# Performance work log

Measured on AMD Instinct MI355X. Metric: run time of the kernel, lower is better.

The kernel has to match this reference:

```python
import jax, jax.numpy as jnp
import numpy as np

ATT, WEMB, VIEW, ADIM, EMB = 312, 512, 16, 2048, 2048
B = 2048
IN = ATT + WEMB + VIEW * WEMB  # 9016; output_dim defaults to input_dim
EPS = 1e-8  # torch cosine_similarity eps


def setup_inputs() -> dict:
    key = jax.random.key(0)
    ks = jax.random.split(key, 8)
    s = 0.02
    return {
        "x": jax.random.normal(ks[0], (B, IN), dtype=jnp.float32),
        "Wq": s * jax.random.normal(ks[1], (WEMB, ADIM), dtype=jnp.float32),
        "bq": jnp.zeros((ADIM,), jnp.float32),
        "Wk": s * jax.random.normal(ks[2], (WEMB, ADIM), dtype=jnp.float32),
        "bk": jnp.zeros((ADIM,), jnp.float32),
        "Wv": s * jax.random.normal(ks[3], (WEMB, ADIM), dtype=jnp.float32),
        "bv": jnp.zeros((ADIM,), jnp.float32),
        "Wm": s * jax.random.normal(ks[4], (ATT + ADIM, EMB), dtype=jnp.float32),
        "bm": jnp.zeros((EMB,), jnp.float32),
        "Wd1": s * jax.random.normal(ks[5], (EMB, 4096), dtype=jnp.float32),
        "bd1": jnp.zeros((4096,), jnp.float32),
        "Wd2": s * jax.random.normal(ks[6], (4096, IN), dtype=jnp.float32),
        "bd2": jnp.zeros((IN,), jnp.float32),
    }


def reference(x, Wq, bq, Wk, bk, Wv, bv, Wm, bm, Wd1, bd1, Wd2, bd2):
    att_emb = x[:, :ATT]                                   # [B, 312]
    desc_emb = x[:, ATT:ATT + WEMB]                        # [B, 512]
    gpt_emb = x[:, ATT + WEMB:].reshape(x.shape[0], -1, WEMB)  # [B, V, 512]

    # q is the same projected desc for every view (expand before linear)
    q = desc_emb @ Wq + bq                                 # [B, A]
    k = jnp.einsum("bvw,wa->bva", gpt_emb, Wk) + bk        # [B, V, A]
    v = jnp.einsum("bvw,wa->bva", gpt_emb, Wv) + bv        # [B, V, A]

    # cosed score: cosine similarity * L2 distance
    dot = jnp.einsum("bva,ba->bv", k, q)                   # [B, V]
    qn = jnp.maximum(jnp.linalg.norm(q, axis=-1), EPS)     # [B]
    kn = jnp.maximum(jnp.linalg.norm(k, axis=-1), EPS)     # [B, V]
    cs = dot / (qn[:, None] * kn)
    ed = jnp.linalg.norm(q[:, None, :] - k, axis=-1)       # [B, V]
    attn = jax.nn.softmax(cs * ed, axis=-1)                # [B, V]

    # torch.matmul([B,V], [B,V,A]) -> [B,B,A]; .mean(dim=1) averages over the
    # attn-batch axis, i.e. fused[j] = mean_b(attn[b]) @ v[j]. Compute the
    # mathematically identical form without the BxBxA intermediate.
    attn_mean = attn.mean(axis=0)                          # [V]
    fused = jnp.einsum("v,bva->ba", attn_mean, v)          # [B, A]

    z = jax.nn.relu(jnp.concatenate([att_emb, fused], axis=1) @ Wm + bm)  # [B, EMB]
    h = jax.nn.relu(z @ Wd1 + bd1)                          # [B, 4096]
    return h @ Wd2 + bd2                                    # [B, IN]
```

## Files before the change

### kernel.cpp

```cpp
#include <hip/hip_runtime.h>


typedef __bf16 bf16x8 __attribute__((ext_vector_type(8)));
typedef float  f32x4  __attribute__((ext_vector_type(4)));
typedef unsigned short u16;

#define ATT   312
#define WEMB  512
#define VIEW  16
#define ADIM  2048
#define EMB   2048
#define BATCH 2048
#define INDIM 9016
#define KCAT  2360
#define KCATP 2432
#define NOUT  9016
#define NOUTP 9216

__device__ __forceinline__ u16 f2bf(float f) {
  unsigned u = __builtin_bit_cast(unsigned, f);
  u += 0x7FFFu + ((u >> 16) & 1u);
  return (u16)(u >> 16);
}

__device__ __forceinline__ void gl_lds16(const u16* g, u16* l) {
  __builtin_amdgcn_global_load_lds((const __attribute__((address_space(1))) void*)g,
                                   (__attribute__((address_space(3))) void*)l, 16, 0, 0);
}

__global__ void castx_k(const float* __restrict__ x, u16* __restrict__ cc,
                        u16* __restrict__ desc, u16* __restrict__ gpt) {
  const int b = blockIdx.x, t = threadIdx.x;
  const float4* row = (const float4*)(x + (size_t)b * INDIM);
  for (int c = t; c < INDIM / 4; c += 256) {
    float4 v = row[c];
    ushort4 o = make_ushort4(f2bf(v.x), f2bf(v.y), f2bf(v.z), f2bf(v.w));
    if (c < ATT / 4)                 *(ushort4*)&cc[(size_t)b * KCATP + c * 4] = o;
    else if (c < (ATT + WEMB) / 4)   *(ushort4*)&desc[(size_t)b * WEMB + (c - ATT / 4) * 4] = o;
    else                             *(ushort4*)&gpt[(size_t)b * (VIEW * WEMB) + (c - (ATT + WEMB) / 4) * 4] = o;
  }
  if (t < (KCATP - KCAT) / 4) {
    *(ushort4*)&cc[(size_t)b * KCATP + KCAT + t * 4] = make_ushort4(0, 0, 0, 0);
  }
}

struct TcDesc { const float* src; u16* dst; int K, N, Kp, Np, ntx, base; };
struct TcArgs { TcDesc d[6]; };

__global__ void transcast6_k(TcArgs A) {
  __shared__ float tile[64][65];
  int mi = 0;
  const int bid = blockIdx.x;
#pragma unroll
  for (int i = 1; i < 6; ++i) if (bid >= A.d[i].base) mi = i;
  const TcDesc& D = A.d[mi];
  const int local = bid - D.base;
  const int n0 = (local % D.ntx) * 64, k0 = (local / D.ntx) * 64;
  const int t = threadIdx.x;
  const int tr = t >> 4, tc4 = (t & 15) * 4;
#pragma unroll
  for (int i = 0; i < 4; ++i) {
    const int k = k0 + tr + i * 16;
    float v0 = 0.f, v1 = 0.f, v2 = 0.f, v3 = 0.f;
    if (k < D.K) {
      const int n = n0 + tc4;
      const float* p = D.src + (size_t)k * D.N + n;
      if (n + 3 < D.N) { float4 v = *(const float4*)p; v0 = v.x; v1 = v.y; v2 = v.z; v3 = v.w; }
      else {
        if (n + 0 < D.N) v0 = p[0];
        if (n + 1 < D.N) v1 = p[1];
        if (n + 2 < D.N) v2 = p[2];
        if (n + 3 < D.N) v3 = p[3];
      }
    }
    tile[tr + i * 16][tc4 + 0] = v0;
    tile[tr + i * 16][tc4 + 1] = v1;
    tile[tr + i * 16][tc4 + 2] = v2;
    tile[tr + i * 16][tc4 + 3] = v3;
  }
  __syncthreads();
#pragma unroll
  for (int i = 0; i < 4; ++i) {
    const int rn = tr + i * 16;
    const int n = n0 + rn;
    const int kk = k0 + tc4;
    if (n < D.Np && kk < D.Kp) {
      const bool nv = (n < D.N);
      ushort4 o = make_ushort4(f2bf(nv ? tile[tc4 + 0][rn] : 0.f),
                               f2bf(nv ? tile[tc4 + 1][rn] : 0.f),
                               f2bf(nv ? tile[tc4 + 2][rn] : 0.f),
                               f2bf(nv ? tile[tc4 + 3][rn] : 0.f));
      *(ushort4*)&D.dst[(size_t)n * D.Kp + kk] = o;
    }
  }
}

__device__ __forceinline__ void stage_half(const u16* __restrict__ src, int ld,
                                           u16* dst, int wave, int lane) {
#pragma unroll
  for (int j = 0; j < 2; ++j) {
    const int s = wave * 2 + j;
    const int r = ((s >> 1) << 4) + (lane >> 2);
    const int c = ((s & 1) << 5) +
                  (((lane & 3) << 3) ^ (((lane >> 5) & 1) << 4));
    gl_lds16(src + (long)r * ld + c, dst + s * 512 + (lane << 3));
  }
}

#define BAR   __builtin_amdgcn_s_barrier()
#define LGKM0 asm volatile("s_waitcnt lgkmcnt(0)" ::: "memory")
#define VM6   asm volatile("s_waitcnt vmcnt(6)" ::: "memory")
#define VM4   asm volatile("s_waitcnt vmcnt(4)" ::: "memory")
#define VM0   asm volatile("s_waitcnt vmcnt(0)" ::: "memory")

#define RDA(bufo, lo, hi) do { _Pragma("unroll") for (int mf = (lo); mf <= (hi); ++mf) \
  _Pragma("unroll") for (int kk = 0; kk < 2; ++kk) \
    a[mf][kk] = *(const bf16x8*)&lds[(bufo) + aoff0 + (mf * 2 + kk) * 512]; } while (0)
#define RDB(bufo, lo, hi) do { _Pragma("unroll") for (int nf = (lo); nf <= (hi); ++nf) \
  _Pragma("unroll") for (int kk = 0; kk < 2; ++kk) \
    b[nf][kk] = *(const bf16x8*)&lds[(bufo) + boff0 + nf * 1024 + kk * 512]; } while (0)
#define QUAD(qm, qn) do { __builtin_amdgcn_s_setprio(1); \
  _Pragma("unroll") for (int m4 = 0; m4 < 4; ++m4) \
  _Pragma("unroll") for (int n2 = 0; n2 < 2; ++n2) \
  _Pragma("unroll") for (int kk = 0; kk < 2; ++kk) \
    acc[(qm) * 4 + m4][(qn) * 2 + n2] = __builtin_amdgcn_mfma_f32_16x16x32_bf16( \
        a[(qm) * 4 + m4][kk], b[(qn) * 2 + n2][kk], acc[(qm) * 4 + m4][(qn) * 2 + n2], 0, 0, 0); \
  __builtin_amdgcn_s_setprio(0); } while (0)

template <int MODE, bool RELU>
__global__ __launch_bounds__(512, 2)
void gemm256(const u16* __restrict__ A, const u16* __restrict__ BT,
             const float* __restrict__ bias, int K, int Nreal,
             float* __restrict__ dstF, u16* __restrict__ dstH,
             float* __restrict__ PF, int ldc,
             const float* __restrict__ qbuf, float* __restrict__ dotb,
             float* __restrict__ kn2b, int mt, int nt, int fastm,
             int ks, int kl) {
  __shared__ alignas(16) u16 lds[65536];
  const int nwg = mt * nt * ks;
  const int xcd = blockIdx.x & 7, idx = blockIdx.x >> 3;
  const int qq = nwg >> 3, rr = nwg & 7;
  const int wg = (xcd < rr ? xcd * (qq + 1) : rr * (qq + 1) + (xcd - rr) * qq) + idx;
  const int ksl = wg % ks;
  const int rem = wg / ks;
  int tm, tn;
  if (fastm) { tm = rem % mt; tn = rem / mt; } else { tn = rem % nt; tm = rem / nt; }

  const int tid = threadIdx.x;
  const int wave = tid >> 6, lane = tid & 63;
  const long m0 = (long)tm * 256, n0 = (long)tn * 256;
  const int wm = wave >> 2, wn = wave & 3;
  const u16* Ab = A + m0 * K + (long)ksl * kl;
  const u16* Bb = BT + n0 * K + (long)ksl * kl;

  f32x4 acc[8][4] = {};
  bf16x8 a[8][2], b[4][2];
  const int LP = (lane & 15) * 32 + ((((lane >> 4) << 3)) ^ (((lane >> 3) & 1) << 4));
  const int aoff0 = wm * 8192 + LP;
  const int boff0 = 16384 + (wn >> 1) * 8192 + (wn & 1) * 4096 + LP;
  const int NT = kl >> 6;

  stage_half(Ab,                K, &lds[0],     wave, lane);
  stage_half(Ab + 128 * K,      K, &lds[8192],  wave, lane);
  stage_half(Bb,                K, &lds[16384], wave, lane);
  stage_half(Bb + 128 * K,      K, &lds[24576], wave, lane);
  stage_half(Ab + 64,           K, &lds[32768], wave, lane);
  stage_half(Ab + 128 * K + 64, K, &lds[40960], wave, lane);
  stage_half(Bb + 64,           K, &lds[49152], wave, lane);
  VM6; BAR;

  const int iters = NT >> 1;
  for (int i = 0; i < iters; ++i) {
    const int t0 = 2 * i;
    const bool nl = (i < iters - 1);
    RDA(0, 0, 3); RDB(0, 0, 1);
    stage_half(Bb + 128 * K + (t0 + 1) * 64, K, &lds[57344], wave, lane);
    BAR; LGKM0; QUAD(0, 0); BAR;
    RDA(0, 4, 7);
    BAR; LGKM0; QUAD(1, 0); BAR;
    RDB(0, 2, 3);
    if (nl) stage_half(Ab + (t0 + 2) * 64, K, &lds[0], wave, lane);
    BAR; LGKM0; QUAD(0, 1); BAR;
    if (nl) stage_half(Ab + 128 * K + (t0 + 2) * 64, K, &lds[8192], wave, lane);
    BAR; QUAD(1, 1);
    if (nl) { VM4; } else { VM0; }
    BAR;
    RDA(32768, 0, 3); RDB(32768, 0, 1);
    if (nl) stage_half(Bb + (t0 + 2) * 64, K, &lds[16384], wave, lane);
    BAR; LGKM0; QUAD(0, 0); BAR;
    RDA(32768, 4, 7);
    if (nl) stage_half(Bb + 128 * K + (t0 + 2) * 64, K, &lds[24576], wave, lane);
    BAR; LGKM0; QUAD(1, 0); BAR;
    RDB(32768, 2, 3);
    if (nl) stage_half(Ab + (t0 + 3) * 64, K, &lds[32768], wave, lane);
    BAR; LGKM0; QUAD(0, 1); BAR;
    if (nl) {
      stage_half(Ab + 128 * K + (t0 + 3) * 64, K, &lds[40960], wave, lane);
      stage_half(Bb + (t0 + 3) * 64, K, &lds[49152], wave, lane);
    }
    BAR; QUAD(1, 1);
    if (nl) VM6;
    BAR;
  }

  const int lr = lane >> 4, lc = lane & 15;
  if (MODE == 2) {
#pragma unroll
    for (int mf = 0; mf < 8; ++mf) {
#pragma unroll
      for (int r = 0; r < 4; ++r) {
        const long grow = m0 + wm * 128 + mf * 16 + lr * 4 + r;
        const long bb = grow >> 4;
        float ds = 0.f, ks2 = 0.f;
#pragma unroll
        for (int nf = 0; nf < 4; ++nf) {
          const long col = n0 + wn * 64 + nf * 16 + lc;
          float kv = acc[mf][nf][r] + bias[col];
          ds += kv * qbuf[bb * ADIM + col];
          ks2 += kv * kv;
        }
#pragma unroll
        for (int m = 1; m < 16; m <<= 1) {
          ds += __shfl_xor(ds, m, 64);
          ks2 += __shfl_xor(ks2, m, 64);
        }
        if (lc == 0) {
          atomicAdd(&dotb[grow], ds);
          atomicAdd(&kn2b[grow], ks2);
        }
      }
    }
  } else if (MODE == 4) {
    float* base = (ksl == 0) ? dstF : PF;
#pragma unroll
    for (int mf = 0; mf < 8; ++mf) {
#pragma unroll
      for (int nf = 0; nf < 4; ++nf) {
        const long col = n0 + wn * 64 + nf * 16 + lc;
        if (col < Nreal) {
          const float bv_ = (ksl == 0) ? bias[col] : 0.f;
#pragma unroll
          for (int r = 0; r < 4; ++r) {
            const long row = m0 + wm * 128 + mf * 16 + lr * 4 + r;
            base[row * (long)ldc + col] = acc[mf][nf][r] + bv_;
          }
        }
      }
    }
  } else {
#pragma unroll
    for (int mf = 0; mf < 8; ++mf) {
#pragma unroll
      for (int nf = 0; nf < 4; ++nf) {
        const long col = n0 + wn * 64 + nf * 16 + lc;
        if (col < Nreal) {
          const float bv_ = bias[col];
#pragma unroll
          for (int r = 0; r < 4; ++r) {
            const long row = m0 + wm * 128 + mf * 16 + lr * 4 + r;
            float v = acc[mf][nf][r] + bv_;
            if (RELU) v = fmaxf(v, 0.f);
            if (MODE == 0) dstF[row * (long)ldc + col] = v;
            else           dstH[row * (long)ldc + col] = f2bf(v);
          }
        }
      }
    }
  }
}

__global__ void addf_k(float* __restrict__ out, const float* __restrict__ p) {
  const size_t i = ((size_t)blockIdx.x * 256 + threadIdx.x) * 4;
  float4 a = *(float4*)&out[i];
  float4 b = *(const float4*)&p[i];
  a.x += b.x; a.y += b.y; a.z += b.z; a.w += b.w;
  *(float4*)&out[i] = a;
}

template <int MODE, bool RELU>
__global__ __launch_bounds__(256, 2)
void gemm_bt(const u16* __restrict__ A, const u16* __restrict__ BT,
             const float* __restrict__ bias, int K, int Nreal,
             float* __restrict__ dstF, u16* __restrict__ dstH, int ldc,
             int mt, int nt, int fastm) {
  __shared__ alignas(16) u16 Ash[128 * 64];
  __shared__ alignas(16) u16 Bsh[128 * 64];
  const int nwg = mt * nt;
  const int xcd = blockIdx.x & 7, idx = blockIdx.x >> 3;
  const int qq = nwg >> 3, rr = nwg & 7;
  const int wg = (xcd < rr ? xcd * (qq + 1) : rr * (qq + 1) + (xcd - rr) * qq) + idx;
  int tm, tn;
  if (fastm) { tm = wg % mt; tn = wg / mt; } else { tn = wg % nt; tm = wg / nt; }

  const int tid = threadIdx.x;
  const int wave = tid >> 6, lane = tid & 63;
  const long m0 = (long)tm * 128;
  const long n0 = (long)tn * 128;
  const int wm = wave >> 1, wnn = wave & 1;
  f32x4 acc[4][4] = {};

  const int srow = (wave << 5) + (lane >> 3);
  const int scol = (lane & 7) << 3;

  for (int k0 = 0; k0 < K; k0 += 64) {
    __syncthreads();
#pragma unroll
    for (int i = 0; i < 4; ++i) {
      const int r = srow + i * 8;
      gl_lds16(A + (m0 + r) * (long)K + k0 + scol, &Ash[r * 64 + scol]);
      gl_lds16(BT + (n0 + r) * (long)K + k0 + scol, &Bsh[r * 64 + scol]);
    }
    __syncthreads();
#pragma unroll
    for (int kb = 0; kb < 2; ++kb) {
      bf16x8 af[4], bfv[4];
#pragma unroll
      for (int f = 0; f < 4; ++f) {
        af[f]  = *(const bf16x8*)&Ash[(wm * 64 + f * 16 + (lane & 15)) * 64 + kb * 32 + (lane >> 4) * 8];
        bfv[f] = *(const bf16x8*)&Bsh[(wnn * 64 + f * 16 + (lane & 15)) * 64 + kb * 32 + (lane >> 4) * 8];
      }
#pragma unroll
      for (int mf = 0; mf < 4; ++mf)
#pragma unroll
        for (int nf = 0; nf < 4; ++nf)
          acc[mf][nf] = __builtin_amdgcn_mfma_f32_16x16x32_bf16(af[mf], bfv[nf], acc[mf][nf], 0, 0, 0);
    }
  }

  const int lr = lane >> 4, lc = lane & 15;
#pragma unroll
  for (int mf = 0; mf < 4; ++mf) {
#pragma unroll
    for (int nf = 0; nf < 4; ++nf) {
      const long col = n0 + wnn * 64 + nf * 16 + lc;
      if (col < Nreal) {
        const float bv_ = bias[col];
#pragma unroll
        for (int r = 0; r < 4; ++r) {
          const long row = m0 + wm * 64 + mf * 16 + lr * 4 + r;
          float v = acc[mf][nf][r] + bv_;
          if (RELU) v = fmaxf(v, 0.f);
          if (MODE == 0) dstF[row * (long)ldc + col] = v;
          else           dstH[row * (long)ldc + col] = f2bf(v);
        }
      }
    }
  }
}

__global__ void qnorm_k(const float* __restrict__ q, float* __restrict__ qn2) {
  const int b = blockIdx.x, t = threadIdx.x;
  const float4* row = (const float4*)(q + (size_t)b * ADIM);
  float s = 0.f;
#pragma unroll
  for (int i = 0; i < 2; ++i) {
    float4 v = row[t + i * 256];
    s += v.x * v.x + v.y * v.y + v.z * v.z + v.w * v.w;
  }
#pragma unroll
  for (int m = 1; m < 64; m <<= 1) s += __shfl_xor(s, m, 64);
  __shared__ float wsum[4];
  if ((t & 63) == 0) wsum[t >> 6] = s;
  __syncthreads();
  if (t == 0) qn2[b] = wsum[0] + wsum[1] + wsum[2] + wsum[3];
}

__global__ void attn_k(const float* __restrict__ dotb, const float* __restrict__ kn2b,
                       const float* __restrict__ qn2, float* __restrict__ asum) {
  const int b = blockIdx.x * 256 + threadIdx.x;
  const int lane = threadIdx.x & 63;
  const float q2 = qn2[b];
  const float qn = fmaxf(sqrtf(q2), 1e-8f);
  float lg[VIEW];
  float mx = -1e30f;
#pragma unroll
  for (int v = 0; v < VIEW; ++v) {
    const float d = dotb[b * VIEW + v], k2 = kn2b[b * VIEW + v];
    const float kn = fmaxf(sqrtf(k2), 1e-8f);
    const float cs = d / (qn * kn);
    const float ed = sqrtf(fmaxf(q2 - 2.f * d + k2, 0.f));
    lg[v] = cs * ed;
    mx = fmaxf(mx, lg[v]);
  }
  float s = 0.f;
#pragma unroll
  for (int v = 0; v < VIEW; ++v) { lg[v] = expf(lg[v] - mx); s += lg[v]; }
  const float inv = 1.f / s;
#pragma unroll
  for (int v = 0; v < VIEW; ++v) {
    float aa = lg[v] * inv;
#pragma unroll
    for (int m = 1; m < 64; m <<= 1) aa += __shfl_xor(aa, m, 64);
    if (lane == 0) atomicAdd(&asum[v], aa);
  }
}

__global__ void gtilde_k(const u16* __restrict__ gpt, const float* __restrict__ asum,
                         u16* __restrict__ g) {
  const int b = blockIdx.x, t = threadIdx.x;
  float am[VIEW];
#pragma unroll
  for (int v = 0; v < VIEW; ++v) am[v] = asum[v] * (1.f / (float)BATCH);
  float s[8] = {};
  const u16* gx = gpt + (size_t)b * (VIEW * WEMB) + t * 8;
#pragma unroll
  for (int v = 0; v < VIEW; ++v) {
    bf16x8 gv = *(const bf16x8*)&gx[v * WEMB];
#pragma unroll
    for (int j = 0; j < 8; ++j) s[j] += am[v] * (float)gv[j];
  }
  ushort4 o0, o1;
  o0 = make_ushort4(f2bf(s[0]), f2bf(s[1]), f2bf(s[2]), f2bf(s[3]));
  o1 = make_ushort4(f2bf(s[4]), f2bf(s[5]), f2bf(s[6]), f2bf(s[7]));
  *(ushort4*)&g[(size_t)b * WEMB + t * 8] = o0;
  *(ushort4*)&g[(size_t)b * WEMB + t * 8 + 4] = o1;
}

extern "C" void kernel_launch(void* const* d_in, const int* in_sizes, int n_in,
                              void* d_out, int out_size, void* d_ws, size_t ws_size,
                              hipStream_t stream) {
  const float* x   = (const float*)d_in[0];
  const float* Wq  = (const float*)d_in[1];
  const float* bq  = (const float*)d_in[2];
  const float* Wk  = (const float*)d_in[3];
  const float* bk  = (const float*)d_in[4];
  const float* Wv  = (const float*)d_in[5];
  const float* bv  = (const float*)d_in[6];
  const float* Wm  = (const float*)d_in[7];
  const float* bm  = (const float*)d_in[8];
  const float* Wd1 = (const float*)d_in[9];
  const float* bd1 = (const float*)d_in[10];
  const float* Wd2 = (const float*)d_in[11];
  const float* bd2 = (const float*)d_in[12];
  float* out = (float*)d_out;

  char* ws = (char*)d_ws;
  size_t off = 0;
  auto alloc = [&](size_t bytes) -> void* {
    void* p = ws + off;
    off = (off + bytes + 255) & ~(size_t)255;
    return p;
  };
  u16* WqT  = (u16*)alloc((size_t)ADIM * WEMB * 2);
  u16* WkT  = (u16*)alloc((size_t)ADIM * WEMB * 2);
  u16* WvT  = (u16*)alloc((size_t)ADIM * WEMB * 2);
  u16* WmT  = (u16*)alloc((size_t)EMB * KCATP * 2);
  u16* Wd1T = (u16*)alloc((size_t)4096 * EMB * 2);
  u16* Wd2T = (u16*)alloc((size_t)NOUTP * 4096 * 2);
  u16* desc = (u16*)alloc((size_t)BATCH * WEMB * 2);
  u16* gpt  = (u16*)alloc((size_t)BATCH * VIEW * WEMB * 2);
  u16* cc   = (u16*)alloc((size_t)BATCH * KCATP * 2);
  float* q    = (float*)alloc((size_t)BATCH * ADIM * 4);
  float* qn2  = (float*)alloc((size_t)BATCH * 4);
  float* stats = (float*)alloc((size_t)(BATCH * VIEW * 2 + 64) * 4);
  float* dotb = stats;
  float* kn2b = stats + BATCH * VIEW;
  float* asum = stats + BATCH * VIEW * 2;
  u16* gt = (u16*)alloc((size_t)BATCH * WEMB * 2);
  u16* z  = (u16*)alloc((size_t)BATCH * EMB * 2);
  (void)alloc((size_t)1 << 20);
  u16* h  = (u16*)alloc((size_t)BATCH * 4096 * 2);
  if (off > ws_size) return;
  float* Pout = (float*)desc;

  hipMemsetAsync(stats, 0, (size_t)(BATCH * VIEW * 2 + 64) * 4, stream);

  castx_k<<<BATCH, 256, 0, stream>>>(x, cc, desc, gpt);

  TcArgs ta;
  int base = 0;
  auto setd = [&](int i, const float* s, u16* d, int K, int N, int Kp, int Np) {
    ta.d[i] = TcDesc{s, d, K, N, Kp, Np, (Np + 63) / 64, base};
    base += ((Np + 63) / 64) * ((Kp + 63) / 64);
  };
  setd(0, Wq, WqT, WEMB, ADIM, WEMB, ADIM);
  setd(1, Wk, WkT, WEMB, ADIM, WEMB, ADIM);
  setd(2, Wv, WvT, WEMB, ADIM, WEMB, ADIM);
  setd(3, Wm, WmT, KCAT, EMB, KCATP, EMB);
  setd(4, Wd1, Wd1T, EMB, 4096, EMB, 4096);
  setd(5, Wd2, Wd2T, 4096, NOUT, 4096, NOUTP);
  transcast6_k<<<base, 256, 0, stream>>>(ta);

  gemm_bt<0, false><<<16 * 16, 256, 0, stream>>>(
      desc, WqT, bq, WEMB, ADIM, q, nullptr, ADIM, BATCH / 128, ADIM / 128, 0);
  qnorm_k<<<BATCH, 256, 0, stream>>>(q, qn2);
  gemm256<2, false><<<128 * 8, 512, 0, stream>>>(
      gpt, WkT, bk, WEMB, ADIM, nullptr, nullptr, nullptr, 0, q, dotb, kn2b,
      BATCH * VIEW / 256, ADIM / 256, 0, 1, WEMB);
  attn_k<<<BATCH / 256, 256, 0, stream>>>(dotb, kn2b, qn2, asum);
  gtilde_k<<<BATCH, 64, 0, stream>>>(gpt, asum, gt);
  gemm_bt<1, false><<<16 * 16, 256, 0, stream>>>(
      gt, WvT, bv, WEMB, ADIM, nullptr, cc + ATT, KCATP, BATCH / 128, ADIM / 128, 0);
  gemm_bt<1, true><<<16 * 16, 256, 0, stream>>>(
      cc, WmT, bm, KCATP, EMB, nullptr, z, EMB, BATCH / 128, EMB / 128, 0);
  gemm256<1, true><<<8 * 16, 512, 0, stream>>>(
      z, Wd1T, bd1, EMB, 4096, nullptr, h, nullptr, 4096, nullptr, nullptr, nullptr,
      BATCH / 256, 4096 / 256, 1, 1, EMB);
  gemm256<4, false><<<8 * 36 * 2, 512, 0, stream>>>(
      h, Wd2T, bd2, 4096, NOUT, out, nullptr, Pout, NOUT, nullptr, nullptr, nullptr,
      BATCH / 256, NOUTP / 256, 1, 2, 2048);
  addf_k<<<(BATCH * NOUT) / 1024, 256, 0, stream>>>(out, Pout);
}
```

Measured before the change: 690.4 us.

## Rebalance decoder GEMM work splits: split-K Wd1, tail-only split-K for Wd2

The first decoder GEMM (z@Wd1) now runs as a 2-way split-K over 256 workgroups instead of 128, writing bf16 partials plus an fp32 partial buffer that a new kernel sums, applies ReLU to, and casts. The second decoder GEMM drops its uniform 2-way split-K. It now computes the 256 full-K tiles for columns below 8192 directly, and splits only the ragged tail column block 8-way in K, reducing it with a small tail kernel. This removes the full-output partial add pass and balances workgroups against the CU count. In exchange it adds an extra kernel, a bf16-rounded intermediate for h's first partial, and larger partial buffers.

```diff
diff --git a/kernel.cpp b/kernel.cpp
--- a/kernel.cpp
+++ b/kernel.cpp
@@ -21,6 +21,10 @@
   unsigned u = __builtin_bit_cast(unsigned, f);
   u += 0x7FFFu + ((u >> 16) & 1u);
   return (u16)(u >> 16);
+}
+__device__ __forceinline__ float bf2f(u16 b) {
+  unsigned u = (unsigned)b << 16;
+  return __builtin_bit_cast(float, u);
 }
 
 __device__ __forceinline__ void gl_lds16(const u16* g, u16* l) {
@@ -127,38 +131,55 @@
         a[(qm) * 4 + m4][kk], b[(qn) * 2 + n2][kk], acc[(qm) * 4 + m4][(qn) * 2 + n2], 0, 0, 0); \
   __builtin_amdgcn_s_setprio(0); } while (0)
 
-template <int MODE, bool RELU>
+template <int MODE>
 __global__ __launch_bounds__(512, 2)
 void gemm256(const u16* __restrict__ A, const u16* __restrict__ BT,
              const float* __restrict__ bias, int K, int Nreal,
              float* __restrict__ dstF, u16* __restrict__ dstH,
              float* __restrict__ PF, int ldc,
              const float* __restrict__ qbuf, float* __restrict__ dotb,
-             float* __restrict__ kn2b, int mt, int nt, int fastm,
-             int ks, int kl) {
+             float* __restrict__ kn2b, int mt, int nt, int fastm) {
   __shared__ alignas(16) u16 lds[65536];
-  const int nwg = mt * nt * ks;
-  const int xcd = blockIdx.x & 7, idx = blockIdx.x >> 3;
-  const int qq = nwg >> 3, rr = nwg & 7;
-  const int wg = (xcd < rr ? xcd * (qq + 1) : rr * (qq + 1) + (xcd - rr) * qq) + idx;
-  const int ksl = wg % ks;
-  const int rem = wg / ks;
-  int tm, tn;
-  if (fastm) { tm = rem % mt; tn = rem / mt; } else { tn = rem % nt; tm = rem / nt; }
+  int tm, tn, ksl = 0, kloc = K;
+  long koff = 0;
+  if (MODE == 5) {
+    if ((int)blockIdx.x < 256) {
+      const int w = ((blockIdx.x & 7) << 5) + (blockIdx.x >> 3);
+      tm = w & 7; tn = w >> 3;
+    } else {
+      const int b2 = blockIdx.x - 256;
+      const int w = ((b2 & 7) << 5) + (b2 >> 3);
+      const int tile = w >> 3; ksl = w & 7;
+      tm = tile & 7; tn = 32 + (tile >> 3);
+      kloc = 512; koff = (long)ksl * 512;
+    }
+  } else if (MODE == 6) {
+    const int w = ((blockIdx.x & 7) << 5) + (blockIdx.x >> 3);
+    ksl = w & 1;
+    const int tile = w >> 1;
+    tm = tile & 7; tn = tile >> 3;
+    kloc = K >> 1; koff = (long)ksl * kloc;
+  } else {
+    const int nwg = mt * nt;
+    const int xcd = blockIdx.x & 7, idx = blockIdx.x >> 3;
+    const int qq = nwg >> 3, rr = nwg & 7;
+    const int wg = (xcd < rr ? xcd * (qq + 1) : rr * (qq + 1) + (xcd - rr) * qq) + idx;
+    if (fastm) { tm = wg % mt; tn = wg / mt; } else { tn = wg % nt; tm = wg / nt; }
+  }
 
   const int tid = threadIdx.x;
   const int wave = tid >> 6, lane = tid & 63;
   const long m0 = (long)tm * 256, n0 = (long)tn * 256;
   const int wm = wave >> 2, wn = wave & 3;
-  const u16* Ab = A + m0 * K + (long)ksl * kl;
-  const u16* Bb = BT + n0 * K + (long)ksl * kl;
+  const u16* Ab = A + m0 * K + koff;
+  const u16* Bb = BT + n0 * K + koff;
 
   f32x4 acc[8][4] = {};
   bf16x8 a[8][2], b[4][2];
   const int LP = (lane & 15) * 32 + ((((lane >> 4) << 3)) ^ (((lane >> 3) & 1) << 4));
   const int aoff0 = wm * 8192 + LP;
   const int boff0 = 16384 + (wn >> 1) * 8192 + (wn & 1) * 4096 + LP;
-  const int NT = kl >> 6;
+  const int NT = kloc >> 6;
 
   stage_half(Ab,                K, &lds[0],     wave, lane);
   stage_half(Ab + 128 * K,      K, &lds[8192],  wave, lane);
@@ -230,51 +251,83 @@
         }
       }
     }
-  } else if (MODE == 4) {
-    float* base = (ksl == 0) ? dstF : PF;
+  } else if (MODE == 5) {
+    if (ksl == 0) {
+#pragma unroll
+      for (int mf = 0; mf < 8; ++mf) {
+#pragma unroll
+        for (int nf = 0; nf < 4; ++nf) {
+          const long col = n0 + wn * 64 + nf * 16 + lc;
+          if (col < Nreal) {
+            const float bv_ = bias[col];
+#pragma unroll
+            for (int r = 0; r < 4; ++r) {
+              const long row = m0 + wm * 128 + mf * 16 + lr * 4 + r;
+              dstF[row * (long)ldc + col] = acc[mf][nf][r] + bv_;
+            }
+          }
+        }
+      }
+    } else {
+      float* pt = PF + (long)(ksl - 1) * BATCH * 1024;
+#pragma unroll
+      for (int mf = 0; mf < 8; ++mf) {
+#pragma unroll
+        for (int nf = 0; nf < 4; ++nf) {
+          const long col = n0 + wn * 64 + nf * 16 + lc;
+#pragma unroll
+          for (int r = 0; r < 4; ++r) {
+            const long row = m0 + wm * 128 + mf * 16 + lr * 4 + r;
+            pt[row * 1024 + (col - 8192)] = acc[mf][nf][r];
+          }
+        }
+      }
+    }
+  } else {
 #pragma unroll
     for (int mf = 0; mf < 8; ++mf) {
 #pragma unroll
       for (int nf = 0; nf < 4; ++nf) {
         const long col = n0 + wn * 64 + nf * 16 + lc;
-        if (col < Nreal) {
-          const float bv_ = (ksl == 0) ? bias[col] : 0.f;
-#pragma unroll
-          for (int r = 0; r < 4; ++r) {
-            const long row = m0 + wm * 128 + mf * 16 + lr * 4 + r;
-            base[row * (long)ldc + col] = acc[mf][nf][r] + bv_;
-          }
-        }
-      }
-    }
-  } else {
-#pragma unroll
-    for (int mf = 0; mf < 8; ++mf) {
-#pragma unroll
-      for (int nf = 0; nf < 4; ++nf) {
-        const long col = n0 + wn * 64 + nf * 16 + lc;
-        if (col < Nreal) {
-          const float bv_ = bias[col];
-#pragma unroll
-          for (int r = 0; r < 4; ++r) {
-            const long row = m0 + wm * 128 + mf * 16 + lr * 4 + r;
-            float v = acc[mf][nf][r] + bv_;
-            if (RELU) v = fmaxf(v, 0.f);
-            if (MODE == 0) dstF[row * (long)ldc + col] = v;
-            else           dstH[row * (long)ldc + col] = f2bf(v);
-          }
-        }
-      }
-    }
-  }
-}
-
-__global__ void addf_k(float* __restrict__ out, const float* __restrict__ p) {
-  const size_t i = ((size_t)blockIdx.x * 256 + threadIdx.x) * 4;
-  float4 a = *(float4*)&out[i];
-  float4 b = *(const float4*)&p[i];
-  a.x += b.x; a.y += b.y; a.z += b.z; a.w += b.w;
-  *(float4*)&out[i] = a;
+        const float bv_ = bias[col];
+#pragma unroll
+        for (int r = 0; r < 4; ++r) {
+          const long row = m0 + wm * 128 + mf * 16 + lr * 4 + r;
+          if (ksl == 0) dstH[row * (long)ldc + col] = f2bf(acc[mf][nf][r] + bv_);
+          else          PF[row * (long)ldc + col] = acc[mf][nf][r];
+        }
+      }
+    }
+  }
+}
+
+__global__ void relucast2_k(u16* __restrict__ h, const float* __restrict__ ph) {
+  const size_t i = ((size_t)blockIdx.x * 256 + threadIdx.x) * 8;
+  bf16x8 hv = *(const bf16x8*)&h[i];
+  float4 pa = *(const float4*)&ph[i];
+  float4 pb = *(const float4*)&ph[i + 4];
+  ushort4 o0 = make_ushort4(f2bf(fmaxf((float)hv[0] + pa.x, 0.f)),
+                            f2bf(fmaxf((float)hv[1] + pa.y, 0.f)),
+                            f2bf(fmaxf((float)hv[2] + pa.z, 0.f)),
+                            f2bf(fmaxf((float)hv[3] + pa.w, 0.f)));
+  ushort4 o1 = make_ushort4(f2bf(fmaxf((float)hv[4] + pb.x, 0.f)),
+                            f2bf(fmaxf((float)hv[5] + pb.y, 0.f)),
+                            f2bf(fmaxf((float)hv[6] + pb.z, 0.f)),
+                            f2bf(fmaxf((float)hv[7] + pb.w, 0.f)));
+  *(ushort4*)&h[i] = o0;
+  *(ushort4*)&h[i + 4] = o1;
+}
+
+__global__ void tailred_k(float* __restrict__ out, const float* __restrict__ pt) {
+  const int i = blockIdx.x * 256 + threadIdx.x;
+  const int row = i / 206, c = (i % 206) * 4;
+  float4 acc = *(float4*)&out[(size_t)row * NOUT + 8192 + c];
+#pragma unroll
+  for (int s = 0; s < 7; ++s) {
+    float4 p = *(const float4*)&pt[(size_t)s * BATCH * 1024 + (size_t)row * 1024 + c];
+    acc.x += p.x; acc.y += p.y; acc.z += p.z; acc.w += p.w;
+  }
+  *(float4*)&out[(size_t)row * NOUT + 8192 + c] = acc;
 }
 
 template <int MODE, bool RELU>
@@ -458,10 +511,10 @@
   float* asum = stats + BATCH * VIEW * 2;
   u16* gt = (u16*)alloc((size_t)BATCH * WEMB * 2);
   u16* z  = (u16*)alloc((size_t)BATCH * EMB * 2);
-  (void)alloc((size_t)1 << 20);
   u16* h  = (u16*)alloc((size_t)BATCH * 4096 * 2);
   if (off > ws_size) return;
-  float* Pout = (float*)desc;
+  float* Ph    = (float*)desc;
+  float* Ptail = (float*)desc;
 
   hipMemsetAsync(stats, 0, (size_t)(BATCH * VIEW * 2 + 64) * 4, stream);
 
@@ -484,20 +537,21 @@
   gemm_bt<0, false><<<16 * 16, 256, 0, stream>>>(
       desc, WqT, bq, WEMB, ADIM, q, nullptr, ADIM, BATCH / 128, ADIM / 128, 0);
   qnorm_k<<<BATCH, 256, 0, stream>>>(q, qn2);
-  gemm256<2, false><<<128 * 8, 512, 0, stream>>>(
+  gemm256<2><<<128 * 8, 512, 0, stream>>>(
       gpt, WkT, bk, WEMB, ADIM, nullptr, nullptr, nullptr, 0, q, dotb, kn2b,
-      BATCH * VIEW / 256, ADIM / 256, 0, 1, WEMB);
+      BATCH * VIEW / 256, ADIM / 256, 0);
   attn_k<<<BATCH / 256, 256, 0, stream>>>(dotb, kn2b, qn2, asum);
   gtilde_k<<<BATCH, 64, 0, stream>>>(gpt, asum, gt);
   gemm_bt<1, false><<<16 * 16, 256, 0, stream>>>(
       gt, WvT, bv, WEMB, ADIM, nullptr, cc + ATT, KCATP, BATCH / 128, ADIM / 128, 0);
   gemm_bt<1, true><<<16 * 16, 256, 0, stream>>>(
       cc, WmT, bm, KCATP, EMB, nullptr, z, EMB, BATCH / 128, EMB / 128, 0);
-  gemm256<1, true><<<8 * 16, 512, 0, stream>>>(
-      z, Wd1T, bd1, EMB, 4096, nullptr, h, nullptr, 4096, nullptr, nullptr, nullptr,
-      BATCH / 256, 4096 / 256, 1, 1, EMB);
-  gemm256<4, false><<<8 * 36 * 2, 512, 0, stream>>>(
-      h, Wd2T, bd2, 4096, NOUT, out, nullptr, Pout, NOUT, nullptr, nullptr, nullptr,
-      BATCH / 256, NOUTP / 256, 1, 2, 2048);
-  addf_k<<<(BATCH * NOUT) / 1024, 256, 0, stream>>>(out, Pout);
-}
+  gemm256<6><<<256, 512, 0, stream>>>(
+      z, Wd1T, bd1, EMB, 4096, nullptr, h, Ph, 4096, nullptr, nullptr, nullptr,
+      0, 0, 0);
+  relucast2_k<<<(BATCH * 4096) / 2048, 256, 0, stream>>>(h, Ph);
+  gemm256<5><<<512, 512, 0, stream>>>(
+      h, Wd2T, bd2, 4096, NOUT, out, nullptr, Ptail, NOUT, nullptr, nullptr, nullptr,
+      0, 0, 0);
+  tailred_k<<<(BATCH * 206 * 4) / 1024, 256, 0, stream>>>(out, Ptail);
+}
```

Result: faster. 658.4 us (-4.6%).
